# Kernel tuning notes

Measured on AMD Instinct MI355X. Metric: run time of the kernel, lower is better.

Reference implementation:

```python
import jax, jax.numpy as jnp
import numpy as np

N_NODES = 100000
N_EDGES = 1600000
EPS = 1e-5
ALPHA = 0.01  # leaky relu slope


def gcn_conv(x, src, dst, W, b, n_nodes):
    """PyG GCNConv: h = W x, add self-loops, out = D^-1/2 (A+I) D^-1/2 h + b."""
    h = x @ W  # [N, d_out]
    # add self loops
    loop = jnp.arange(n_nodes, dtype=src.dtype)
    s = jnp.concatenate([src, loop])
    d = jnp.concatenate([dst, loop])
    # symmetric normalization: deg computed at destination over A + I
    deg = jax.ops.segment_sum(jnp.ones_like(d, dtype=h.dtype), d, num_segments=n_nodes)
    dinv = jnp.where(deg > 0, jax.lax.rsqrt(deg), 0.0)
    norm = dinv[s] * dinv[d]  # [E+N]
    msg = h[s] * norm[:, None]  # gather + scale (memory bound)
    out = jax.ops.segment_sum(msg, d, num_segments=n_nodes)
    return out + b


def batch_norm(x, gamma, beta):
    mu = jnp.mean(x, axis=0)
    var = jnp.var(x, axis=0)
    return (x - mu) * jax.lax.rsqrt(var + EPS) * gamma + beta


def setup_inputs() -> dict:
    key = jax.random.key(0)
    ks = jax.random.split(key, 6)
    emb = jax.random.normal(ks[0], (N_NODES, 64), dtype=jnp.float32)
    edge_index = jax.random.randint(ks[1], (2, N_EDGES), 0, N_NODES, dtype=jnp.int32)
    W1 = jax.random.normal(ks[2], (64, 128), dtype=jnp.float32) * 0.05
    W2 = jax.random.normal(ks[3], (128, 256), dtype=jnp.float32) * 0.05
    Wf = jax.random.normal(ks[4], (256, 256), dtype=jnp.float32) * 0.05
    return {
        "embeddings": emb, "edge_index": edge_index,
        "W1": W1, "b1": jnp.zeros((128,), jnp.float32),
        "g1": jnp.ones((128,), jnp.float32), "beta1": jnp.zeros((128,), jnp.float32),
        "W2": W2, "b2": jnp.zeros((256,), jnp.float32),
        "g2": jnp.ones((256,), jnp.float32), "beta2": jnp.zeros((256,), jnp.float32),
        "Wf": Wf, "bf": jnp.zeros((256,), jnp.float32),
    }


def reference(embeddings, edge_index, W1, b1, g1, beta1, W2, b2, g2, beta2, Wf, bf):
    src, dst = edge_index[0], edge_index[1]
    x = gcn_conv(embeddings, src, dst, W1, b1, N_NODES)
    x = batch_norm(x, g1, beta1)
    x = jnp.where(x >= 0, x, ALPHA * x)  # leaky relu; dropout = identity (eval)
    x = gcn_conv(x, src, dst, W2, b2, N_NODES)
    x = batch_norm(x, g2, beta2)
    x = jnp.where(x >= 0, x, ALPHA * x)
    return x @ Wf + bf
```

## Files before the change

kernel.cpp:

```cpp
#include <hip/hip_runtime.h>

#define NN 100000
#define NE 1600000
constexpr float EPS_BN = 1e-5f;
constexpr float ALPHA = 0.01f;
constexpr int NBUCK = (NN + 127) / 128;
constexpr int GA = 128;
constexpr int EPB = NE / GA;
constexpr int GX = (NN + 63) / 64;

typedef __attribute__((ext_vector_type(8))) short short8;
typedef __attribute__((ext_vector_type(4))) float f32x4;

__device__ __forceinline__ float bfu2f(uint lo16) {
    union { uint i; float f; } v; v.i = lo16 << 16; return v.f;
}
__device__ __forceinline__ float bfhi2f(uint u) {
    union { uint i; float f; } v; v.i = u & 0xffff0000u; return v.f;
}
__device__ __forceinline__ ushort f2bf(float f) {
    union { float f; uint i; } v; v.f = f;
    return (ushort)((v.i + 0x7fffu + ((v.i >> 16) & 1u)) >> 16);
}

__global__ __launch_bounds__(256) void k_bhist(const int* __restrict__ dstv, int* __restrict__ bcnt) {
    __shared__ int hist[NBUCK];
    for (int i = threadIdx.x; i < NBUCK; i += 256) hist[i] = 0;
    __syncthreads();
    int base = blockIdx.x * EPB;
    for (int i = threadIdx.x; i < EPB; i += 256)
        atomicAdd(&hist[dstv[base + i] >> 7], 1);
    __syncthreads();
    for (int i = threadIdx.x; i < NBUCK; i += 256)
        bcnt[blockIdx.x * NBUCK + i] = hist[i];
}

__global__ __launch_bounds__(256) void k_btot(const int* __restrict__ bcnt, int* __restrict__ tot) {
    int b = blockIdx.x * 256 + threadIdx.x;
    if (b < NBUCK) {
        int t = 0;
        for (int k = 0; k < GA; ++k) t += bcnt[k * NBUCK + b];
        tot[b] = t;
    }
}

__global__ __launch_bounds__(1024) void k_bscanT(const int* __restrict__ tot, int* __restrict__ bbase) {
    __shared__ int tmp[1024];
    int b = threadIdx.x;
    int v = (b < NBUCK) ? tot[b] : 0;
    tmp[b] = v;
    __syncthreads();
    for (int off = 1; off < 1024; off <<= 1) {
        int u = (b >= off) ? tmp[b - off] : 0;
        __syncthreads();
        tmp[b] += u;
        __syncthreads();
    }
    if (b < NBUCK) bbase[b] = tmp[b] - v;
    if (b == 0) bbase[NBUCK] = NE;
}

__global__ __launch_bounds__(256) void k_bcur(const int* __restrict__ bcnt, const int* __restrict__ bbase,
                                              int* __restrict__ gcur) {
    int b = blockIdx.x * 256 + threadIdx.x;
    if (b < NBUCK) {
        int cur = bbase[b];
        for (int k = 0; k < GA; ++k) { gcur[k * NBUCK + b] = cur; cur += bcnt[k * NBUCK + b]; }
    }
}

__global__ __launch_bounds__(256) void k_bscatter(const int* __restrict__ srcv, const int* __restrict__ dstv,
                                                  const int* __restrict__ gcur, uint* __restrict__ bpair) {
    __shared__ int lcur[NBUCK];
    for (int i = threadIdx.x; i < NBUCK; i += 256) lcur[i] = gcur[blockIdx.x * NBUCK + i];
    __syncthreads();
    int base = blockIdx.x * EPB;
    for (int i = threadIdx.x; i < EPB; i += 256) {
        int d = dstv[base + i], s = srcv[base + i];
        int slot = atomicAdd(&lcur[d >> 7], 1);
        bpair[slot] = ((uint)(d & 127) << 17) | (uint)s;
    }
}

__global__ __launch_bounds__(256) void k_bcsr(const uint* __restrict__ bpair, const int* __restrict__ bbase,
                                              int* __restrict__ col, int* __restrict__ cnt,
                                              int* __restrict__ indptr, float* __restrict__ dinv) {
    __shared__ int h[128];
    __shared__ int off[128];
    int b = blockIdx.x, t = threadIdx.x;
    int p0 = bbase[b], p1 = bbase[b + 1];
    if (t < 128) h[t] = 0;
    __syncthreads();
    for (int i = p0 + t; i < p1; i += 256)
        atomicAdd(&h[bpair[i] >> 17], 1);
    __syncthreads();
    if (t < 128) off[t] = h[t];
    __syncthreads();
    for (int o = 1; o < 128; o <<= 1) {
        int u = 0;
        if (t < 128 && t >= o) u = off[t - o];
        __syncthreads();
        if (t < 128) off[t] += u;
        __syncthreads();
    }
    if (t < 128) {
        int st = p0 + off[t] - h[t];
        int node = b * 128 + t;
        if (node < NN) {
            indptr[node] = st;
            cnt[node] = h[t];
            dinv[node] = rsqrtf((float)(h[t] + 1));
        }
        off[t] = st;
    }
    __syncthreads();
    for (int i = p0 + t; i < p1; i += 256) {
        uint u = bpair[i];
        int slot = atomicAdd(&off[u >> 17], 1);
        col[slot] = (int)(u & 0x1FFFFu);
    }
}

__global__ void k_wtrans_all(const float* __restrict__ W1, const float* __restrict__ W2,
                             const float* __restrict__ Wf, ushort* __restrict__ w1t,
                             ushort* __restrict__ w2t, ushort* __restrict__ wft) {
    int i = blockIdx.x * 256 + threadIdx.x;
    if (i < 8192) {
        int m = i / 64, k = i % 64;
        w1t[i] = f2bf(W1[(size_t)k * 128 + m]);
    } else if (i < 8192 + 32768) {
        int j = i - 8192;
        int m = j / 128, k = j % 128;
        w2t[j] = f2bf(W2[(size_t)k * 256 + m]);
    } else if (i < 8192 + 32768 + 65536) {
        int j = i - 8192 - 32768;
        int m = j / 256, k = j % 256;
        wft[j] = f2bf(Wf[(size_t)k * 256 + m]);
    }
}

__global__ __launch_bounds__(256) void k_semb(const float* __restrict__ emb, const float* __restrict__ dinv,
                                              uint2* __restrict__ embs) {
    int i = blockIdx.x * 256 + threadIdx.x;
    if (i >= NN * 16) return;
    int row = i >> 4;
    float dn = dinv[row];
    float4 f = ((const float4*)emb)[i];
    uint2 o;
    o.x = (uint)f2bf(f.x * dn) | ((uint)f2bf(f.y * dn) << 16);
    o.y = (uint)f2bf(f.z * dn) | ((uint)f2bf(f.w * dn) << 16);
    embs[i] = o;
}

__global__ __launch_bounds__(256) void k_x2s(const ushort* __restrict__ H1, const float* __restrict__ sc,
                                             const float* __restrict__ sh, const float* __restrict__ dinv,
                                             ushort* __restrict__ x2s) {
    int i = blockIdx.x * 256 + threadIdx.x;
    if (i >= NN * 16) return;
    int row = i >> 4, f0 = (i & 15) * 8;
    float dn = dinv[row];
    uint4 u = ((const uint4*)H1)[i];
    uint uu[4] = {u.x, u.y, u.z, u.w};
    uint oo[4];
#pragma unroll
    for (int q = 0; q < 4; ++q) {
        int f = f0 + q * 2;
        float e0 = bfu2f(uu[q] & 0xffffu) * sc[f] + sh[f];
        float e1 = bfhi2f(uu[q]) * sc[f + 1] + sh[f + 1];
        e0 = ((e0 >= 0.f) ? e0 : ALPHA * e0) * dn;
        e1 = ((e1 >= 0.f) ? e1 : ALPHA * e1) * dn;
        oo[q] = (uint)f2bf(e0) | ((uint)f2bf(e1) << 16);
    }
    uint4 o; o.x = oo[0]; o.y = oo[1]; o.z = oo[2]; o.w = oo[3];
    ((uint4*)x2s)[i] = o;
}

__global__ __launch_bounds__(64) void k_agg64(const ushort* __restrict__ X, const int* __restrict__ indptr,
                                              const int* __restrict__ cnt, const int* __restrict__ col,
                                              const float* __restrict__ dinv, ushort* __restrict__ out) {
    int n = blockIdx.x, t = threadIdx.x;
    int t2 = t & 31, h = t >> 5;
    __shared__ int sc[64];
    int start = indptr[n], c = cnt[n];
    const uint* Xu = (const uint*)X;
    float a0 = 0.f, a1 = 0.f;
    if (h == 0) {
        uint u = Xu[(size_t)n * 32 + t2];
        a0 = bfu2f(u & 0xffffu); a1 = bfhi2f(u);
    }
    for (int base = 0; base < c; base += 64) {
        int m = min(64, c - base);
        if (t < m) sc[t] = col[start + base + t];
        __syncthreads();
#pragma unroll 2
        for (int j = h; j < m; j += 2) {
            uint v = Xu[(size_t)sc[j] * 32 + t2];
            a0 += bfu2f(v & 0xffffu); a1 += bfhi2f(v);
        }
        __syncthreads();
    }
    a0 += __shfl_xor(a0, 32);
    a1 += __shfl_xor(a1, 32);
    if (h == 0) {
        float dn = dinv[n];
        ((uint*)out)[(size_t)n * 32 + t2] = (uint)f2bf(a0 * dn) | ((uint)f2bf(a1 * dn) << 16);
    }
}

__global__ __launch_bounds__(64) void k_agg128(const ushort* __restrict__ X, const int* __restrict__ indptr,
                                               const int* __restrict__ cnt, const int* __restrict__ col,
                                               const float* __restrict__ dinv, ushort* __restrict__ out) {
    int n = blockIdx.x, t = threadIdx.x;
    __shared__ int sc[64];
    int start = indptr[n], c = cnt[n];
    const uint* Xu = (const uint*)X;
    uint u = Xu[(size_t)n * 64 + t];
    float a0 = bfu2f(u & 0xffffu), a1 = bfhi2f(u);
    float b0 = 0.f, b1 = 0.f;
    for (int base = 0; base < c; base += 64) {
        int m = min(64, c - base);
        if (t < m) sc[t] = col[start + base + t];
        __syncthreads();
        int j = 0;
#pragma unroll 2
        for (; j + 2 <= m; j += 2) {
            uint v0 = Xu[(size_t)sc[j] * 64 + t];
            uint v1 = Xu[(size_t)sc[j + 1] * 64 + t];
            a0 += bfu2f(v0 & 0xffffu); a1 += bfhi2f(v0);
            b0 += bfu2f(v1 & 0xffffu); b1 += bfhi2f(v1);
        }
        if (j < m) {
            uint v = Xu[(size_t)sc[j] * 64 + t];
            a0 += bfu2f(v & 0xffffu); a1 += bfhi2f(v);
        }
        __syncthreads();
    }
    a0 += b0; a1 += b1;
    float dn = dinv[n];
    ((uint*)out)[(size_t)n * 64 + t] = (uint)f2bf(a0 * dn) | ((uint)f2bf(a1 * dn) << 16);
}

template <int AT>
__device__ __forceinline__ uint4 xform8(uint4 u, int kbase, const float* s_sc, const float* s_sh) {
    if constexpr (AT == 1) {
        uint uu[4] = {u.x, u.y, u.z, u.w};
        uint oo[4];
#pragma unroll
        for (int q = 0; q < 4; ++q) {
            int kq = kbase + q * 2;
            float e0 = bfu2f(uu[q] & 0xffffu) * s_sc[kq] + s_sh[kq];
            float e1 = bfhi2f(uu[q]) * s_sc[kq + 1] + s_sh[kq + 1];
            e0 = (e0 >= 0.f) ? e0 : ALPHA * e0;
            e1 = (e1 >= 0.f) ? e1 : ALPHA * e1;
            oo[q] = (uint)f2bf(e0) | ((uint)f2bf(e1) << 16);
        }
        return make_uint4(oo[0], oo[1], oo[2], oo[3]);
    } else {
        return u;
    }
}

template <int K, int NOUT, int AT, int OUT, bool STATS>
__global__ __launch_bounds__(256) void k_mgemm(
        const void* __restrict__ Ap, const ushort* __restrict__ BT, void* __restrict__ Cp,
        const float* __restrict__ scale, const float* __restrict__ shift,
        const float* __restrict__ bias, float* __restrict__ partials) {
    constexpr int BM = 64, BK = 32, LDA = 40;
    constexpr int WN = NOUT / 4;
    constexpr int NF = WN / 16;
    constexpr int NT = K / BK;
    __shared__ ushort As[2][BM * LDA];
    __shared__ float s_sc[K];
    __shared__ float s_sh[K];

    int tid = threadIdx.x;
    int brow = blockIdx.x * BM;
    int lane = tid & 63, wid = tid >> 6;
    int fr = lane & 15, fq = lane >> 4;
    int fk = fq * 8;

    const int srow = tid >> 2, sk0 = (tid & 3) * 8;
    const int grow = brow + srow;
    const bool aok = grow < NN;
    const ushort* arp = (const ushort*)Ap + (size_t)grow * K + sk0;

    if constexpr (AT == 1) {
        for (int i = tid; i < K; i += 256) { s_sc[i] = scale[i]; s_sh[i] = shift[i]; }
        __syncthreads();
    }

    f32x4 acc[4][NF];
#pragma unroll
    for (int mi = 0; mi < 4; ++mi)
#pragma unroll
        for (int ni = 0; ni < NF; ++ni) acc[mi][ni] = (f32x4){0.f, 0.f, 0.f, 0.f};

    uint4 av = make_uint4(0, 0, 0, 0);
    if (aok) av = *(const uint4*)arp;
    av = xform8<AT>(av, sk0, s_sc, s_sh);
    *(uint4*)&As[0][srow * LDA + sk0] = av;

    for (int t = 0; t < NT; ++t) {
        __syncthreads();
        uint4 anext = make_uint4(0, 0, 0, 0);
        if (t + 1 < NT && aok)
            anext = *(const uint4*)(arp + (t + 1) * BK);

        short8 bfv[NF];
#pragma unroll
        for (int ni = 0; ni < NF; ++ni)
            bfv[ni] = *(const short8*)(BT + (size_t)(wid * WN + ni * 16 + fr) * K + t * BK + fk);

        short8 af[4];
#pragma unroll
        for (int mi = 0; mi < 4; ++mi)
            af[mi] = *(const short8*)&As[t & 1][(mi * 16 + fr) * LDA + fk];

#pragma unroll
        for (int mi = 0; mi < 4; ++mi)
#pragma unroll
            for (int ni = 0; ni < NF; ++ni)
                acc[mi][ni] = __builtin_amdgcn_mfma_f32_16x16x32_bf16(af[mi], bfv[ni], acc[mi][ni], 0, 0, 0);

        if (t + 1 < NT) {
            anext = xform8<AT>(anext, (t + 1) * BK + sk0, s_sc, s_sh);
            *(uint4*)&As[(t + 1) & 1][srow * LDA + sk0] = anext;
        }
    }

    float bv[NF];
#pragma unroll
    for (int ni = 0; ni < NF; ++ni) bv[ni] = bias[wid * WN + ni * 16 + fr];

    float sv[NF], qv[NF];
#pragma unroll
    for (int ni = 0; ni < NF; ++ni) { sv[ni] = 0.f; qv[ni] = 0.f; }

#pragma unroll
    for (int mi = 0; mi < 4; ++mi)
#pragma unroll
        for (int r = 0; r < 4; ++r) {
            int row = brow + mi * 16 + fq * 4 + r;
            if (row < NN) {
#pragma unroll
                for (int ni = 0; ni < NF; ++ni) {
                    float x = acc[mi][ni][r] + bv[ni];
                    int c = wid * WN + ni * 16 + fr;
                    if constexpr (OUT == 1)
                        ((float*)Cp)[(size_t)row * NOUT + c] = x;
                    else
                        ((ushort*)Cp)[(size_t)row * NOUT + c] = f2bf(x);
                    if constexpr (STATS) { sv[ni] += x; qv[ni] += x * x; }
                }
            }
        }

    if constexpr (STATS) {
#pragma unroll
        for (int ni = 0; ni < NF; ++ni) {
            sv[ni] += __shfl_down(sv[ni], 32); qv[ni] += __shfl_down(qv[ni], 32);
            sv[ni] += __shfl_down(sv[ni], 16); qv[ni] += __shfl_down(qv[ni], 16);
        }
        if (fq == 0) {
            float* pb = partials + (size_t)blockIdx.x * 2 * NOUT;
#pragma unroll
            for (int ni = 0; ni < NF; ++ni) {
                int c = wid * WN + ni * 16 + fr;
                pb[c] = sv[ni];
                pb[NOUT + c] = qv[ni];
            }
        }
    }
}

template <int M>
__global__ __launch_bounds__(256) void k_bnred(const float* __restrict__ partials, const float* __restrict__ g,
                                               const float* __restrict__ be, float* __restrict__ scale,
                                               float* __restrict__ shift) {
    int tid = threadIdx.x;
    int fl = tid & 15, bl = tid >> 4;
    int f = blockIdx.x * 16 + fl;
    float s = 0.f, q = 0.f;
    for (int b = bl; b < GX; b += 16) {
        s += partials[(size_t)b * 2 * M + f];
        q += partials[(size_t)b * 2 * M + M + f];
    }
    __shared__ float rs[256], rq[256];
    rs[tid] = s; rq[tid] = q;
    __syncthreads();
    for (int h = 128; h >= 16; h >>= 1) {
        if (tid < h) { rs[tid] += rs[tid + h]; rq[tid] += rq[tid + h]; }
        __syncthreads();
    }
    if (tid < 16) {
        float su = rs[tid], qu = rq[tid];
        float mu = su * (1.f / NN);
        float var = qu * (1.f / NN) - mu * mu;
        float r = rsqrtf(var + EPS_BN);
        float sc = g[f] * r;
        scale[f] = sc;
        shift[f] = be[f] - mu * sc;
    }
}

extern "C" void kernel_launch(void* const* d_in, const int* in_sizes, int n_in,
                              void* d_out, int out_size, void* d_ws, size_t ws_size,
                              hipStream_t stream) {
    const float* emb = (const float*)d_in[0];
    const int* eidx  = (const int*)d_in[1];
    const float* W1  = (const float*)d_in[2];
    const float* b1  = (const float*)d_in[3];
    const float* g1  = (const float*)d_in[4];
    const float* be1 = (const float*)d_in[5];
    const float* W2  = (const float*)d_in[6];
    const float* b2  = (const float*)d_in[7];
    const float* g2  = (const float*)d_in[8];
    const float* be2 = (const float*)d_in[9];
    const float* Wf  = (const float*)d_in[10];
    const float* bf  = (const float*)d_in[11];
    float* out = (float*)d_out;
    const int* srcv = eidx;
    const int* dstv = eidx + NE;

    char* w = (char*)d_ws;
    auto alloc = [&](size_t bytes) {
        char* p = w;
        w += (bytes + 255) / 256 * 256;
        return p;
    };
    int* cnt    = (int*)alloc((size_t)NN * 4);
    int* indptr = (int*)alloc((size_t)NN * 4);
    int* bcnt   = (int*)alloc((size_t)NBUCK * GA * 4);
    int* gcur   = (int*)alloc((size_t)NBUCK * GA * 4);
    int* tot    = (int*)alloc((size_t)NBUCK * 4);
    int* bbase  = (int*)alloc((size_t)(NBUCK + 1) * 4);
    int* colb   = (int*)alloc((size_t)NE * 4);
    uint* bpair = (uint*)alloc((size_t)NE * 4);
    float* dinv = (float*)alloc((size_t)NN * 4);
    float* partials = (float*)alloc((size_t)GX * 512 * 4);
    float* sc1 = (float*)alloc(128 * 4);
    float* sh1 = (float*)alloc(128 * 4);
    float* sc2 = (float*)alloc(256 * 4);
    float* sh2 = (float*)alloc(256 * 4);
    ushort* w1t = (ushort*)alloc((size_t)128 * 64 * 2);
    ushort* w2t = (ushort*)alloc((size_t)256 * 128 * 2);
    ushort* wft = (ushort*)alloc((size_t)256 * 256 * 2);
    ushort* slabA = (ushort*)alloc((size_t)NN * 128 * 2);
    ushort* slabB = (ushort*)alloc((size_t)NN * 128 * 2);
    ushort* H2 = (ushort*)alloc((size_t)NN * 256 * 2);

    ushort* embs = slabA;
    ushort* aggE = slabB;
    ushort* H1   = slabA;
    ushort* x2s  = slabB;
    ushort* agg2 = slabA;

    constexpr int GB4 = (NBUCK + 255) / 256;

    k_bhist<<<GA, 256, 0, stream>>>(dstv, bcnt);
    k_btot<<<GB4, 256, 0, stream>>>(bcnt, tot);
    k_bscanT<<<1, 1024, 0, stream>>>(tot, bbase);
    k_bcur<<<GB4, 256, 0, stream>>>(bcnt, bbase, gcur);
    k_bscatter<<<GA, 256, 0, stream>>>(srcv, dstv, gcur, bpair);
    k_bcsr<<<NBUCK, 256, 0, stream>>>(bpair, bbase, colb, cnt, indptr, dinv);

    k_wtrans_all<<<(8192 + 32768 + 65536 + 255) / 256, 256, 0, stream>>>(W1, W2, Wf, w1t, w2t, wft);

    k_semb<<<(NN * 16 + 255) / 256, 256, 0, stream>>>(emb, dinv, (uint2*)embs);
    k_agg64<<<NN, 64, 0, stream>>>(embs, indptr, cnt, colb, dinv, aggE);
    k_mgemm<64, 128, 2, 2, true><<<GX, 256, 0, stream>>>(aggE, w1t, H1, nullptr, nullptr, b1, partials);
    k_bnred<128><<<8, 256, 0, stream>>>(partials, g1, be1, sc1, sh1);

    k_x2s<<<(NN * 16 + 255) / 256, 256, 0, stream>>>(H1, sc1, sh1, dinv, x2s);
    k_agg128<<<NN, 64, 0, stream>>>(x2s, indptr, cnt, colb, dinv, agg2);
    k_mgemm<128, 256, 2, 2, true><<<GX, 256, 0, stream>>>(agg2, w2t, H2, nullptr, nullptr, b2, partials);
    k_bnred<256><<<16, 256, 0, stream>>>(partials, g2, be2, sc2, sh2);

    k_mgemm<256, 256, 1, 1, false><<<GX, 256, 0, stream>>>(H2, wft, out, sc2, sh2, bf, nullptr);
}
```

Measured before the change: 349.5 us.

## Fuse neighbor aggregation into GCN GEMM kernels via shared-memory A tiles

```diff
diff --git a/kernel.cpp b/kernel.cpp
--- a/kernel.cpp
+++ b/kernel.cpp
@@ -175,119 +175,99 @@
     ((uint4*)x2s)[i] = o;
 }
 
-__global__ __launch_bounds__(64) void k_agg64(const ushort* __restrict__ X, const int* __restrict__ indptr,
-                                              const int* __restrict__ cnt, const int* __restrict__ col,
-                                              const float* __restrict__ dinv, ushort* __restrict__ out) {
-    int n = blockIdx.x, t = threadIdx.x;
-    int t2 = t & 31, h = t >> 5;
-    __shared__ int sc[64];
-    int start = indptr[n], c = cnt[n];
-    const uint* Xu = (const uint*)X;
-    float a0 = 0.f, a1 = 0.f;
-    if (h == 0) {
-        uint u = Xu[(size_t)n * 32 + t2];
-        a0 = bfu2f(u & 0xffffu); a1 = bfhi2f(u);
-    }
-    for (int base = 0; base < c; base += 64) {
-        int m = min(64, c - base);
-        if (t < m) sc[t] = col[start + base + t];
-        __syncthreads();
-#pragma unroll 2
-        for (int j = h; j < m; j += 2) {
-            uint v = Xu[(size_t)sc[j] * 32 + t2];
-            a0 += bfu2f(v & 0xffffu); a1 += bfhi2f(v);
-        }
-        __syncthreads();
-    }
-    a0 += __shfl_xor(a0, 32);
-    a1 += __shfl_xor(a1, 32);
-    if (h == 0) {
-        float dn = dinv[n];
-        ((uint*)out)[(size_t)n * 32 + t2] = (uint)f2bf(a0 * dn) | ((uint)f2bf(a1 * dn) << 16);
-    }
-}
-
-__global__ __launch_bounds__(64) void k_agg128(const ushort* __restrict__ X, const int* __restrict__ indptr,
-                                               const int* __restrict__ cnt, const int* __restrict__ col,
-                                               const float* __restrict__ dinv, ushort* __restrict__ out) {
-    int n = blockIdx.x, t = threadIdx.x;
-    __shared__ int sc[64];
-    int start = indptr[n], c = cnt[n];
-    const uint* Xu = (const uint*)X;
-    uint u = Xu[(size_t)n * 64 + t];
-    float a0 = bfu2f(u & 0xffffu), a1 = bfhi2f(u);
-    float b0 = 0.f, b1 = 0.f;
-    for (int base = 0; base < c; base += 64) {
-        int m = min(64, c - base);
-        if (t < m) sc[t] = col[start + base + t];
-        __syncthreads();
-        int j = 0;
-#pragma unroll 2
-        for (; j + 2 <= m; j += 2) {
-            uint v0 = Xu[(size_t)sc[j] * 64 + t];
-            uint v1 = Xu[(size_t)sc[j + 1] * 64 + t];
-            a0 += bfu2f(v0 & 0xffffu); a1 += bfhi2f(v0);
-            b0 += bfu2f(v1 & 0xffffu); b1 += bfhi2f(v1);
-        }
-        if (j < m) {
-            uint v = Xu[(size_t)sc[j] * 64 + t];
-            a0 += bfu2f(v & 0xffffu); a1 += bfhi2f(v);
-        }
-        __syncthreads();
-    }
-    a0 += b0; a1 += b1;
-    float dn = dinv[n];
-    ((uint*)out)[(size_t)n * 64 + t] = (uint)f2bf(a0 * dn) | ((uint)f2bf(a1 * dn) << 16);
-}
-
-template <int AT>
-__device__ __forceinline__ uint4 xform8(uint4 u, int kbase, const float* s_sc, const float* s_sh) {
-    if constexpr (AT == 1) {
-        uint uu[4] = {u.x, u.y, u.z, u.w};
-        uint oo[4];
-#pragma unroll
-        for (int q = 0; q < 4; ++q) {
-            int kq = kbase + q * 2;
-            float e0 = bfu2f(uu[q] & 0xffffu) * s_sc[kq] + s_sh[kq];
-            float e1 = bfhi2f(uu[q]) * s_sc[kq + 1] + s_sh[kq + 1];
-            e0 = (e0 >= 0.f) ? e0 : ALPHA * e0;
-            e1 = (e1 >= 0.f) ? e1 : ALPHA * e1;
-            oo[q] = (uint)f2bf(e0) | ((uint)f2bf(e1) << 16);
-        }
-        return make_uint4(oo[0], oo[1], oo[2], oo[3]);
-    } else {
-        return u;
-    }
-}
-
-template <int K, int NOUT, int AT, int OUT, bool STATS>
-__global__ __launch_bounds__(256) void k_mgemm(
-        const void* __restrict__ Ap, const ushort* __restrict__ BT, void* __restrict__ Cp,
-        const float* __restrict__ scale, const float* __restrict__ shift,
+template <int K, int NOUT, int OUT, bool STATS>
+__global__ __launch_bounds__(256) void k_aggmm(
+        const ushort* __restrict__ X, const int* __restrict__ indptr, const int* __restrict__ cnt,
+        const int* __restrict__ col, const float* __restrict__ dinv,
+        const ushort* __restrict__ BT, void* __restrict__ Cp,
         const float* __restrict__ bias, float* __restrict__ partials) {
-    constexpr int BM = 64, BK = 32, LDA = 40;
+    constexpr int BM = 64, BK = 32, LDA = K + 8;
     constexpr int WN = NOUT / 4;
     constexpr int NF = WN / 16;
     constexpr int NT = K / BK;
-    __shared__ ushort As[2][BM * LDA];
-    __shared__ float s_sc[K];
-    __shared__ float s_sh[K];
+    __shared__ ushort As[BM * LDA];
 
     int tid = threadIdx.x;
     int brow = blockIdx.x * BM;
     int lane = tid & 63, wid = tid >> 6;
     int fr = lane & 15, fq = lane >> 4;
     int fk = fq * 8;
-
-    const int srow = tid >> 2, sk0 = (tid & 3) * 8;
-    const int grow = brow + srow;
-    const bool aok = grow < NN;
-    const ushort* arp = (const ushort*)Ap + (size_t)grow * K + sk0;
-
-    if constexpr (AT == 1) {
-        for (int i = tid; i < K; i += 256) { s_sc[i] = scale[i]; s_sh[i] = shift[i]; }
-        __syncthreads();
-    }
+    const uint* Xu = (const uint*)X;
+
+    if constexpr (K == 128) {
+        for (int ni = 0; ni < 16; ++ni) {
+            int node = brow + wid * 16 + ni;
+            int arow = (wid * 16 + ni) * LDA;
+            if (node < NN) {
+                uint u = Xu[(size_t)node * 64 + lane];
+                float a0 = bfu2f(u & 0xffffu), a1 = bfhi2f(u);
+                float b0 = 0.f, b1 = 0.f;
+                int start = indptr[node], c = cnt[node];
+                for (int base = 0; base < c; base += 64) {
+                    int m = min(64, c - base);
+                    int colv = (lane < m) ? col[start + base + lane] : 0;
+                    int j = 0;
+                    for (; j + 2 <= m; j += 2) {
+                        int s0 = __shfl(colv, j), s1 = __shfl(colv, j + 1);
+                        uint v0 = Xu[(size_t)s0 * 64 + lane];
+                        uint v1 = Xu[(size_t)s1 * 64 + lane];
+                        a0 += bfu2f(v0 & 0xffffu); a1 += bfhi2f(v0);
+                        b0 += bfu2f(v1 & 0xffffu); b1 += bfhi2f(v1);
+                    }
+                    if (j < m) {
+                        int s0 = __shfl(colv, j);
+                        uint v = Xu[(size_t)s0 * 64 + lane];
+                        a0 += bfu2f(v & 0xffffu); a1 += bfhi2f(v);
+                    }
+                }
+                a0 += b0; a1 += b1;
+                float dn = dinv[node];
+                *(uint*)&As[arow + lane * 2] = (uint)f2bf(a0 * dn) | ((uint)f2bf(a1 * dn) << 16);
+            } else {
+                *(uint*)&As[arow + lane * 2] = 0;
+            }
+        }
+    } else {
+        int t2 = lane & 31, h = lane >> 5;
+        for (int ni = 0; ni < 16; ++ni) {
+            int node = brow + wid * 16 + ni;
+            int arow = (wid * 16 + ni) * LDA;
+            if (node < NN) {
+                float a0 = 0.f, a1 = 0.f;
+                if (h == 0) {
+                    uint u = Xu[(size_t)node * 32 + t2];
+                    a0 = bfu2f(u & 0xffffu); a1 = bfhi2f(u);
+                }
+                int start = indptr[node], c = cnt[node];
+                for (int base = 0; base < c; base += 64) {
+                    int m = min(64, c - base);
+                    int colv = (lane < m) ? col[start + base + lane] : 0;
+                    int j = 0;
+                    for (; j + 2 <= m; j += 2) {
+                        int sj = __shfl(colv, j + h);
+                        uint v = Xu[(size_t)sj * 32 + t2];
+                        a0 += bfu2f(v & 0xffffu); a1 += bfhi2f(v);
+                    }
+                    if (j < m) {
+                        int sj = __shfl(colv, j);
+                        if (h == 0) {
+                            uint v = Xu[(size_t)sj * 32 + t2];
+                            a0 += bfu2f(v & 0xffffu); a1 += bfhi2f(v);
+                        }
+                    }
+                }
+                a0 += __shfl_xor(a0, 32);
+                a1 += __shfl_xor(a1, 32);
+                if (h == 0) {
+                    float dn = dinv[node];
+                    *(uint*)&As[arow + t2 * 2] = (uint)f2bf(a0 * dn) | ((uint)f2bf(a1 * dn) << 16);
+                }
+            } else {
+                if (h == 0) *(uint*)&As[arow + t2 * 2] = 0;
+            }
+        }
+    }
+    __syncthreads();
 
     f32x4 acc[4][NF];
 #pragma unroll
@@ -295,37 +275,21 @@
 #pragma unroll
         for (int ni = 0; ni < NF; ++ni) acc[mi][ni] = (f32x4){0.f, 0.f, 0.f, 0.f};
 
-    uint4 av = make_uint4(0, 0, 0, 0);
-    if (aok) av = *(const uint4*)arp;
-    av = xform8<AT>(av, sk0, s_sc, s_sh);
-    *(uint4*)&As[0][srow * LDA + sk0] = av;
-
+#pragma unroll
     for (int t = 0; t < NT; ++t) {
-        __syncthreads();
-        uint4 anext = make_uint4(0, 0, 0, 0);
-        if (t + 1 < NT && aok)
-            anext = *(const uint4*)(arp + (t + 1) * BK);
-
         short8 bfv[NF];
 #pragma unroll
         for (int ni = 0; ni < NF; ++ni)
             bfv[ni] = *(const short8*)(BT + (size_t)(wid * WN + ni * 16 + fr) * K + t * BK + fk);
-
         short8 af[4];
 #pragma unroll
         for (int mi = 0; mi < 4; ++mi)
-            af[mi] = *(const short8*)&As[t & 1][(mi * 16 + fr) * LDA + fk];
-
+            af[mi] = *(const short8*)&As[(mi * 16 + fr) * LDA + t * BK + fk];
 #pragma unroll
         for (int mi = 0; mi < 4; ++mi)
 #pragma unroll
             for (int ni = 0; ni < NF; ++ni)
                 acc[mi][ni] = __builtin_amdgcn_mfma_f32_16x16x32_bf16(af[mi], bfv[ni], acc[mi][ni], 0, 0, 0);
-
-        if (t + 1 < NT) {
-            anext = xform8<AT>(anext, (t + 1) * BK + sk0, s_sc, s_sh);
-            *(uint4*)&As[(t + 1) & 1][srow * LDA + sk0] = anext;
-        }
     }
 
     float bv[NF];
@@ -371,6 +335,104 @@
             }
         }
     }
+}
+
+__device__ __forceinline__ uint4 xformBN(uint4 u, int kbase, const float* s_sc, const float* s_sh) {
+    uint uu[4] = {u.x, u.y, u.z, u.w};
+    uint oo[4];
+#pragma unroll
+    for (int q = 0; q < 4; ++q) {
+        int kq = kbase + q * 2;
+        float e0 = bfu2f(uu[q] & 0xffffu) * s_sc[kq] + s_sh[kq];
+        float e1 = bfhi2f(uu[q]) * s_sc[kq + 1] + s_sh[kq + 1];
+        e0 = (e0 >= 0.f) ? e0 : ALPHA * e0;
+        e1 = (e1 >= 0.f) ? e1 : ALPHA * e1;
+        oo[q] = (uint)f2bf(e0) | ((uint)f2bf(e1) << 16);
+    }
+    return make_uint4(oo[0], oo[1], oo[2], oo[3]);
+}
+
+template <int K, int NOUT>
+__global__ __launch_bounds__(256) void k_mgemm(
+        const ushort* __restrict__ Ap, const ushort* __restrict__ BT, float* __restrict__ Cp,
+        const float* __restrict__ scale, const float* __restrict__ shift,
+        const float* __restrict__ bias) {
+    constexpr int BM = 64, BK = 32, LDA = 40;
+    constexpr int WN = NOUT / 4;
+    constexpr int NF = WN / 16;
+    constexpr int NT = K / BK;
+    __shared__ ushort As[2][BM * LDA];
+    __shared__ float s_sc[K];
+    __shared__ float s_sh[K];
+
+    int tid = threadIdx.x;
+    int brow = blockIdx.x * BM;
+    int lane = tid & 63, wid = tid >> 6;
+    int fr = lane & 15, fq = lane >> 4;
+    int fk = fq * 8;
+
+    const int srow = tid >> 2, sk0 = (tid & 3) * 8;
+    const int grow = brow + srow;
+    const bool aok = grow < NN;
+    const ushort* arp = Ap + (size_t)grow * K + sk0;
+
+    for (int i = tid; i < K; i += 256) { s_sc[i] = scale[i]; s_sh[i] = shift[i]; }
+    __syncthreads();
+
+    f32x4 acc[4][NF];
+#pragma unroll
+    for (int mi = 0; mi < 4; ++mi)
+#pragma unroll
+        for (int ni = 0; ni < NF; ++ni) acc[mi][ni] = (f32x4){0.f, 0.f, 0.f, 0.f};
+
+    uint4 av = make_uint4(0, 0, 0, 0);
+    if (aok) av = *(const uint4*)arp;
+    av = xformBN(av, sk0, s_sc, s_sh);
+    *(uint4*)&As[0][srow * LDA + sk0] = av;
+
+    for (int t = 0; t < NT; ++t) {
+        __syncthreads();
+        uint4 anext = make_uint4(0, 0, 0, 0);
+        if (t + 1 < NT && aok)
+            anext = *(const uint4*)(arp + (t + 1) * BK);
+
+        short8 bfv[NF];
+#pragma unroll
+        for (int ni = 0; ni < NF; ++ni)
+            bfv[ni] = *(const short8*)(BT + (size_t)(wid * WN + ni * 16 + fr) * K + t * BK + fk);
+        short8 af[4];
+#pragma unroll
+        for (int mi = 0; mi < 4; ++mi)
+            af[mi] = *(const short8*)&As[t & 1][(mi * 16 + fr) * LDA + fk];
+#pragma unroll
+        for (int mi = 0; mi < 4; ++mi)
+#pragma unroll
+            for (int ni = 0; ni < NF; ++ni)
+                acc[mi][ni] = __builtin_amdgcn_mfma_f32_16x16x32_bf16(af[mi], bfv[ni], acc[mi][ni], 0, 0, 0);
+
+        if (t + 1 < NT) {
+            anext = xformBN(anext, (t + 1) * BK + sk0, s_sc, s_sh);
+            *(uint4*)&As[(t + 1) & 1][srow * LDA + sk0] = anext;
+        }
+    }
+
+    float bv[NF];
+#pragma unroll
+    for (int ni = 0; ni < NF; ++ni) bv[ni] = bias[wid * WN + ni * 16 + fr];
+
+#pragma unroll
+    for (int mi = 0; mi < 4; ++mi)
+#pragma unroll
+        for (int r = 0; r < 4; ++r) {
+            int row = brow + mi * 16 + fq * 4 + r;
+            if (row < NN) {
+#pragma unroll
+                for (int ni = 0; ni < NF; ++ni) {
+                    int c = wid * WN + ni * 16 + fr;
+                    Cp[(size_t)row * NOUT + c] = acc[mi][ni][r] + bv[ni];
+                }
+            }
+        }
 }
 
 template <int M>
@@ -445,15 +507,10 @@
     ushort* w1t = (ushort*)alloc((size_t)128 * 64 * 2);
     ushort* w2t = (ushort*)alloc((size_t)256 * 128 * 2);
     ushort* wft = (ushort*)alloc((size_t)256 * 256 * 2);
-    ushort* slabA = (ushort*)alloc((size_t)NN * 128 * 2);
-    ushort* slabB = (ushort*)alloc((size_t)NN * 128 * 2);
-    ushort* H2 = (ushort*)alloc((size_t)NN * 256 * 2);
-
-    ushort* embs = slabA;
-    ushort* aggE = slabB;
-    ushort* H1   = slabA;
-    ushort* x2s  = slabB;
-    ushort* agg2 = slabA;
+    ushort* embs = (ushort*)alloc((size_t)NN * 64 * 2);
+    ushort* H1   = (ushort*)alloc((size_t)NN * 128 * 2);
+    ushort* x2s  = (ushort*)alloc((size_t)NN * 128 * 2);
+    ushort* H2   = (ushort*)alloc((size_t)NN * 256 * 2);
 
     constexpr int GB4 = (NBUCK + 255) / 256;
 
@@ -467,14 +524,12 @@
     k_wtrans_all<<<(8192 + 32768 + 65536 + 255) / 256, 256, 0, stream>>>(W1, W2, Wf, w1t, w2t, wft);
 
     k_semb<<<(NN * 16 + 255) / 256, 256, 0, stream>>>(emb, dinv, (uint2*)embs);
-    k_agg64<<<NN, 64, 0, stream>>>(embs, indptr, cnt, colb, dinv, aggE);
-    k_mgemm<64, 128, 2, 2, true><<<GX, 256, 0, stream>>>(aggE, w1t, H1, nullptr, nullptr, b1, partials);
+    k_aggmm<64, 128, 2, true><<<GX, 256, 0, stream>>>(embs, indptr, cnt, colb, dinv, w1t, H1, b1, partials);
     k_bnred<128><<<8, 256, 0, stream>>>(partials, g1, be1, sc1, sh1);
 
     k_x2s<<<(NN * 16 + 255) / 256, 256, 0, stream>>>(H1, sc1, sh1, dinv, x2s);
-    k_agg128<<<NN, 64, 0, stream>>>(x2s, indptr, cnt, colb, dinv, agg2);
-    k_mgemm<128, 256, 2, 2, true><<<GX, 256, 0, stream>>>(agg2, w2t, H2, nullptr, nullptr, b2, partials);
+    k_aggmm<128, 256, 2, true><<<GX, 256, 0, stream>>>(x2s, indptr, cnt, colb, dinv, w2t, H2, b2, partials);
     k_bnred<256><<<16, 256, 0, stream>>>(partials, g2, be2, sc2, sh2);
 
-    k_mgemm<256, 256, 1, 1, false><<<GX, 256, 0, stream>>>(H2, wft, out, sc2, sh2, bf, nullptr);
-}
+    k_mgemm<256, 256><<<GX, 256, 0, stream>>>(H2, wft, out, sc2, sh2, bf);
+}
```

Result: slower. 577.3 us (+65.2%).
